# Kernel optimization log

Measured on AMD Instinct MI355X. Metric: run time of the kernel, lower is better.

## Reference

```python
import jax, jax.numpy as jnp
import numpy as np
import math

B, T, C, H = 2, 2048, 512, 8
K, DIL = 3, 1
EPS = 1e-5


def _ln(x, g, b):
    m = jnp.mean(x, axis=-1, keepdims=True)
    v = jnp.mean(jnp.square(x - m), axis=-1, keepdims=True)
    return (x - m) * jax.lax.rsqrt(v + EPS) * g + b


def setup_inputs() -> dict:
    key = jax.random.key(0)
    ks = jax.random.split(key, 12)
    s = 0.02
    return {
        "x": jax.random.normal(ks[0], (B, T, C), jnp.float32),
        "conv_w": jax.random.normal(ks[1], (C, C, K), jnp.float32) * s,  # OIH
        "conv_b": jax.random.normal(ks[2], (C,), jnp.float32) * s,
        "g1": jnp.ones((C,), jnp.float32), "b1": jnp.zeros((C,), jnp.float32),
        "qkv_w": jax.random.normal(ks[3], (C, 3 * C), jnp.float32) * s,
        "qkv_b": jax.random.normal(ks[4], (3 * C,), jnp.float32) * s,
        "proj_w": jax.random.normal(ks[5], (C, C), jnp.float32) * s,
        "proj_b": jax.random.normal(ks[6], (C,), jnp.float32) * s,
        "g2": jnp.ones((C,), jnp.float32), "b2": jnp.zeros((C,), jnp.float32),
        "ffn_w1": jax.random.normal(ks[7], (C, 2 * C), jnp.float32) * s,
        "ffn_b1": jax.random.normal(ks[8], (2 * C,), jnp.float32) * s,
        "ffn_w2": jax.random.normal(ks[9], (2 * C, C), jnp.float32) * s,
        "ffn_b2": jax.random.normal(ks[10], (C,), jnp.float32) * s,
        "g3": jnp.ones((C,), jnp.float32), "b3": jnp.zeros((C,), jnp.float32),
    }


def reference(x, conv_w, conv_b, g1, b1, qkv_w, qkv_b, proj_w, proj_b,
              g2, b2, ffn_w1, ffn_b1, ffn_w2, ffn_b2, g3, b3):
    b, t, c = x.shape
    hd = c // H
    # --- causal dilated conv (left-pad only == pad both + right-trim) ---
    pad = (K - 1) * DIL
    xc = jnp.transpose(x, (0, 2, 1))  # [B,C,T]
    conv = jax.lax.conv_general_dilated(
        xc, conv_w, window_strides=(1,), padding=[(pad, 0)],
        rhs_dilation=(DIL,), dimension_numbers=("NCH", "OIH", "NCH"))
    conv = conv + conv_b[None, :, None]
    x = _ln(x + jnp.transpose(conv, (0, 2, 1)), g1, b1)
    # --- causal self-attention ---
    qkv = (x @ qkv_w + qkv_b).reshape(b, t, 3, H, hd)
    qkv = jnp.transpose(qkv, (2, 0, 3, 1, 4))  # [3,B,H,T,hd]
    q, k, v = qkv[0], qkv[1], qkv[2]
    scores = jnp.einsum("bhqd,bhkd->bhqk", q, k) / math.sqrt(hd)
    causal = jnp.tril(jnp.ones((t, t), bool))
    scores = jnp.where(causal, scores, -jnp.inf)
    attn = jax.nn.softmax(scores, axis=-1)
    out = jnp.einsum("bhqk,bhkd->bhqd", attn, v)
    out = jnp.transpose(out, (0, 2, 1, 3)).reshape(b, t, c)
    out = out @ proj_w + proj_b
    x = _ln(x + out, g2, b2)
    # --- FFN ---
    ffn = jax.nn.relu(x @ ffn_w1 + ffn_b1) @ ffn_w2 + ffn_b2
    return _ln(x + ffn, g3, b3)
```

## Files before the change

kernel.cpp:

```cpp
#include <hip/hip_runtime.h>
#include <hip/hip_bf16.h>

#define TT 2048

typedef __attribute__((ext_vector_type(4))) float f32x4;
typedef __attribute__((ext_vector_type(8))) __bf16 bf16x8;
typedef __attribute__((ext_vector_type(4))) short short4v;
typedef __attribute__((ext_vector_type(8))) short short8v;

enum { M_CONV = 0, M_QKV = 1, M_PROJ = 2, M_FFN1 = 3, M_FFN2 = 4 };

__device__ __forceinline__ void gload16(const void* g, void* l) {
    __builtin_amdgcn_global_load_lds(
        (__attribute__((address_space(1))) void*)g,
        (__attribute__((address_space(3))) void*)l, 16, 0, 0);
}

__device__ __forceinline__ short f2bf(float f) {
    unsigned u = __float_as_uint(f);
    u = (u + 0x7fffu + ((u >> 16) & 1u)) >> 16;
    return (short)u;
}

__device__ __forceinline__ float bf2f(short s) {
    unsigned u = ((unsigned)(unsigned short)s) << 16;
    return __uint_as_float(u);
}

__global__ __launch_bounds__(256) void prep_all(
    const float* __restrict__ conv_w, const float* __restrict__ x,
    const float* __restrict__ qkv_w, const float* __restrict__ proj_w,
    const float* __restrict__ f1w, const float* __restrict__ f2w,
    short* __restrict__ cwT, short* __restrict__ xpad,
    short* __restrict__ qkvT, short* __restrict__ projT,
    short* __restrict__ f1T, short* __restrict__ f2T) {
    if (blockIdx.x < 2048) {
        int t = blockIdx.x;
        const float* src; short* dst; int K, N, lt;
        if (t < 768)       { src = qkv_w;  dst = qkvT;  K = 512;  N = 1536; lt = t; }
        else if (t < 1024) { src = proj_w; dst = projT; K = 512;  N = 512;  lt = t - 768; }
        else if (t < 1536) { src = f1w;    dst = f1T;   K = 512;  N = 1024; lt = t - 1024; }
        else               { src = f2w;    dst = f2T;   K = 1024; N = 512;  lt = t - 1536; }
        int ntn = N >> 5;
        int kt = lt / ntn, nt = lt - kt * ntn;
        int k0 = kt * 32, n0 = nt * 32;
        __shared__ float tile[32][33];
        int c = threadIdx.x & 31, r = threadIdx.x >> 5;
        #pragma unroll
        for (int i = 0; i < 4; i++)
            tile[r + i * 8][c] = src[(size_t)(k0 + r + i * 8) * N + n0 + c];
        __syncthreads();
        #pragma unroll
        for (int i = 0; i < 4; i++)
            dst[(size_t)(n0 + r + i * 8) * K + k0 + c] = f2bf(tile[c][r + i * 8]);
        return;
    }
    int idx = (blockIdx.x - 2048) * 256 + threadIdx.x;
    if (idx < 786432) {
        int tap = idx >> 18, i = (idx >> 9) & 511, o = idx & 511;
        cwT[(size_t)o * 1536 + tap * 512 + i] = f2bf(conv_w[((size_t)o * 512 + i) * 3 + tap]);
        return;
    }
    idx -= 786432;
    if (idx < 2099200) {
        int i = idx & 511, rp = idx >> 9;
        int bb = rp / 2050, rr = rp - bb * 2050;
        int t = rr - 2;
        float v = (t >= 0) ? x[((size_t)(bb << 11) + t) * 512 + i] : 0.f;
        xpad[((size_t)bb * 2050 + rr) * 512 + i] = f2bf(v);
    }
}

__global__ __launch_bounds__(512) void ln_row(const float* __restrict__ in,
                                              const float* __restrict__ g,
                                              const float* __restrict__ b,
                                              float* __restrict__ outf,
                                              short* __restrict__ outb) {
    int row = blockIdx.x * 8 + (threadIdx.x >> 6);
    int l = threadIdx.x & 63;
    const float* p = in + (size_t)row * 512 + l * 8;
    f32x4 v0 = *(const f32x4*)p;
    f32x4 v1 = *(const f32x4*)(p + 4);
    float s = 0.f, ss = 0.f;
    #pragma unroll
    for (int i = 0; i < 4; i++) { s += v0[i]; ss += v0[i] * v0[i]; }
    #pragma unroll
    for (int i = 0; i < 4; i++) { s += v1[i]; ss += v1[i] * v1[i]; }
    #pragma unroll
    for (int off = 1; off < 64; off <<= 1) {
        s  += __shfl_xor(s, off);
        ss += __shfl_xor(ss, off);
    }
    float mean = s * (1.f / 512);
    float var  = ss * (1.f / 512) - mean * mean;
    float rstd = rsqrtf(var + 1e-5f);
    f32x4 g0 = *(const f32x4*)(g + l * 8), g1 = *(const f32x4*)(g + l * 8 + 4);
    f32x4 b0 = *(const f32x4*)(b + l * 8), b1 = *(const f32x4*)(b + l * 8 + 4);
    f32x4 o0, o1;
    #pragma unroll
    for (int i = 0; i < 4; i++) {
        o0[i] = (v0[i] - mean) * rstd * g0[i] + b0[i];
        o1[i] = (v1[i] - mean) * rstd * g1[i] + b1[i];
    }
    float* q = outf + (size_t)row * 512 + l * 8;
    *(f32x4*)q = o0;
    *(f32x4*)(q + 4) = o1;
    if (outb) {
        short4v p0, p1;
        #pragma unroll
        for (int i = 0; i < 4; i++) { p0[i] = f2bf(o0[i]); p1[i] = f2bf(o1[i]); }
        *(short4v*)(outb + (size_t)row * 512 + l * 8) = p0;
        *(short4v*)(outb + (size_t)row * 512 + l * 8 + 4) = p1;
    }
}

template<int MODE>
__device__ __forceinline__ const short* a_ptr(const short* A, int m0, int r, int kk, int K) {
    if constexpr (MODE == M_CONV) {
        int row = m0 + r;
        int bb = row >> 11, t5 = row & 2047;
        int tap = kk >> 9, k2 = kk & 511;
        return A + ((size_t)(bb * 2050 + t5 + tap) * 512 + k2);
    } else {
        return A + ((size_t)(m0 + r) * K + kk);
    }
}

template<int MODE>
__global__ __launch_bounds__(128) void gemm_mfma(
    const short* __restrict__ A, const short* __restrict__ Bw,
    const float* __restrict__ bias, const float* __restrict__ res,
    void* __restrict__ Cout, short* __restrict__ vTb, int K) {
    __shared__ short As[64 * 64];
    __shared__ short Bs[64 * 64];
    const int tid = threadIdx.x;
    const int w = tid >> 6, l = tid & 63;
    const int lr = l & 15, lc = l >> 4;
    const int m0 = blockIdx.x * 64, n0 = blockIdx.y * 64;
    f32x4 acc[2][4];
    #pragma unroll
    for (int mf = 0; mf < 2; mf++)
        #pragma unroll
        for (int nf = 0; nf < 4; nf++) acc[mf][nf] = (f32x4){0.f, 0.f, 0.f, 0.f};

    for (int k0 = 0; k0 < K; k0 += 64) {
        #pragma unroll
        for (int i = 0; i < 4; i++) {
            int u = i * 128 + tid;
            int r = u >> 3, c = (u & 7) ^ (r & 7);
            gload16(a_ptr<MODE>(A, m0, r, k0 + c * 8, K), (char*)As + u * 16);
            gload16(Bw + ((size_t)(n0 + r) * K + k0 + c * 8), (char*)Bs + u * 16);
        }
        __syncthreads();
        bf16x8 af[2][2], bfv[4][2];
        #pragma unroll
        for (int mf = 0; mf < 2; mf++)
            #pragma unroll
            for (int ks = 0; ks < 2; ks++) {
                int rr = w * 32 + mf * 16 + lr;
                int cc = (ks * 4 + lc) ^ (rr & 7);
                af[mf][ks] = *(const bf16x8*)&As[rr * 64 + cc * 8];
            }
        #pragma unroll
        for (int nf = 0; nf < 4; nf++)
            #pragma unroll
            for (int ks = 0; ks < 2; ks++) {
                int rr = nf * 16 + lr;
                int cc = (ks * 4 + lc) ^ (rr & 7);
                bfv[nf][ks] = *(const bf16x8*)&Bs[rr * 64 + cc * 8];
            }
        __builtin_amdgcn_s_setprio(1);
        #pragma unroll
        for (int nf = 0; nf < 4; nf++)
            #pragma unroll
            for (int ks = 0; ks < 2; ks++)
                #pragma unroll
                for (int mf = 0; mf < 2; mf++)
                    acc[mf][nf] = __builtin_amdgcn_mfma_f32_16x16x32_bf16(
                        af[mf][ks], bfv[nf][ks], acc[mf][nf], 0, 0, 0);
        __builtin_amdgcn_s_setprio(0);
        __syncthreads();
    }
    #pragma unroll
    for (int mf = 0; mf < 2; mf++) {
        int row0 = m0 + w * 32 + mf * 16 + lc * 4;
        #pragma unroll
        for (int nf = 0; nf < 4; nf++) {
            int col = n0 + nf * 16 + lr;
            float bv = bias[col];
            if constexpr (MODE == M_CONV || MODE == M_PROJ || MODE == M_FFN2) {
                float* Cf = (float*)Cout;
                #pragma unroll
                for (int rg = 0; rg < 4; rg++) {
                    size_t off = (size_t)(row0 + rg) * 512 + col;
                    Cf[off] = acc[mf][nf][rg] + bv + res[off];
                }
            } else if constexpr (MODE == M_FFN1) {
                short* Cb = (short*)Cout;
                #pragma unroll
                for (int rg = 0; rg < 4; rg++)
                    Cb[(size_t)(row0 + rg) * 1024 + col] =
                        f2bf(fmaxf(acc[mf][nf][rg] + bv, 0.f));
            } else {
                short* Cb = (short*)Cout;
                float v[4];
                #pragma unroll
                for (int rg = 0; rg < 4; rg++) {
                    v[rg] = acc[mf][nf][rg] + bv;
                    Cb[(size_t)(row0 + rg) * 1536 + col] = f2bf(v[rg]);
                }
                if (col >= 1024) {
                    int vc = col - 1024, hh = vc >> 6, dd = vc & 63;
                    int bb = row0 >> 11, t5 = row0 & 2047;
                    short4v pk = {f2bf(v[0]), f2bf(v[1]), f2bf(v[2]), f2bf(v[3])};
                    *(short4v*)&vTb[((size_t)((bb << 3) + hh) * 64 + dd) * 2048 + t5] = pk;
                }
            }
        }
    }
}

__global__ __launch_bounds__(256) void attn_part(const short* __restrict__ qkvb,
                                                 const short* __restrict__ vTb,
                                                 short* __restrict__ pO,
                                                 float* __restrict__ pML) {
    __shared__ short SM[20992];
    const int tid = threadIdx.x;
    const int w = tid >> 6, l = tid & 63;
    const int lr = l & 15, lc = l >> 4;
    const int L = blockIdx.x;
    const int bh = L & 15;
    const int par = (L >> 4) & 1;
    const int qt = 31 - (L >> 5);
    const int b = bh >> 3, h = bh & 7;
    const int qr = w * 16, q0 = qt * 64;
    const int pbase = 16384 + w * (16 * 72);
    const int ntiles = (qt >= par) ? ((qt - par) >> 1) + 1 : 0;

    #pragma unroll
    for (int i = 0; i < 2; i++) {
        int u = i * 256 + tid, r = u >> 3, c = (u & 7) ^ (r & 7);
        gload16(qkvb + ((size_t)(b * 2048 + q0 + r) * 1536 + h * 64 + c * 8),
                (char*)&SM[16384] + u * 16);
        if (ntiles > 0) {
            gload16(qkvb + ((size_t)(b * 2048 + par * 64 + r) * 1536 + 512 + h * 64 + c * 8),
                    (char*)&SM[0] + u * 16);
            gload16(vTb + ((size_t)(bh * 64 + r) * 2048 + par * 64 + c * 8),
                    (char*)&SM[8192] + u * 16);
        }
    }
    __syncthreads();
    bf16x8 aq[2];
    #pragma unroll
    for (int ks = 0; ks < 2; ks++) {
        int rr = qr + lr;
        int cc = (lc + 4 * ks) ^ (rr & 7);
        aq[ks] = *(const bf16x8*)&SM[16384 + rr * 64 + cc * 8];
    }
    __syncthreads();

    f32x4 o[4];
    float mst[4], lst[4];
    #pragma unroll
    for (int nf = 0; nf < 4; nf++) o[nf] = (f32x4){0.f, 0.f, 0.f, 0.f};
    #pragma unroll
    for (int rg = 0; rg < 4; rg++) { mst[rg] = -1e30f; lst[rg] = 0.f; }

    for (int s = 0; s < ntiles; s++) {
        const int kt = par + 2 * s;
        const int cur = s & 1;
        if (s + 1 < ntiles) {
            int ktn = kt + 2, nb = (cur ^ 1) * 4096;
            #pragma unroll
            for (int i = 0; i < 2; i++) {
                int u = i * 256 + tid, r = u >> 3, c = (u & 7) ^ (r & 7);
                gload16(qkvb + ((size_t)(b * 2048 + ktn * 64 + r) * 1536 + 512 + h * 64 + c * 8),
                        (char*)&SM[nb] + u * 16);
                gload16(vTb + ((size_t)(bh * 64 + r) * 2048 + ktn * 64 + c * 8),
                        (char*)&SM[8192 + nb] + u * 16);
            }
        }
        f32x4 s4[4];
        #pragma unroll
        for (int nf = 0; nf < 4; nf++) s4[nf] = (f32x4){0.f, 0.f, 0.f, 0.f};
        __builtin_amdgcn_s_setprio(1);
        #pragma unroll
        for (int nf = 0; nf < 4; nf++) {
            #pragma unroll
            for (int ks = 0; ks < 2; ks++) {
                int rr = nf * 16 + lr;
                int cc = (lc + 4 * ks) ^ (rr & 7);
                bf16x8 bk = *(const bf16x8*)&SM[cur * 4096 + rr * 64 + cc * 8];
                s4[nf] = __builtin_amdgcn_mfma_f32_16x16x32_bf16(aq[ks], bk, s4[nf], 0, 0, 0);
            }
        }
        __builtin_amdgcn_s_setprio(0);
        const bool diag = (kt == qt);
        #pragma unroll
        for (int nf = 0; nf < 4; nf++) {
            #pragma unroll
            for (int rg = 0; rg < 4; rg++) {
                float v = s4[nf][rg] * 0.125f;
                if (diag && (nf * 16 + lr > qr + lc * 4 + rg)) v = -1e30f;
                s4[nf][rg] = v;
            }
        }
        float rm[4];
        int ok = 1;
        #pragma unroll
        for (int rg = 0; rg < 4; rg++) {
            float m_ = fmaxf(fmaxf(s4[0][rg], s4[1][rg]), fmaxf(s4[2][rg], s4[3][rg]));
            m_ = fmaxf(m_, __shfl_xor(m_, 1));
            m_ = fmaxf(m_, __shfl_xor(m_, 2));
            m_ = fmaxf(m_, __shfl_xor(m_, 4));
            m_ = fmaxf(m_, __shfl_xor(m_, 8));
            rm[rg] = m_;
            ok &= (m_ <= mst[rg] + 8.f);
        }
        if (!__all(ok)) {
            #pragma unroll
            for (int rg = 0; rg < 4; rg++) {
                float mn = fmaxf(mst[rg], rm[rg]);
                float alpha = __expf(mst[rg] - mn);
                mst[rg] = mn;
                lst[rg] *= alpha;
                #pragma unroll
                for (int nf = 0; nf < 4; nf++) o[nf][rg] *= alpha;
            }
        }
        #pragma unroll
        for (int rg = 0; rg < 4; rg++) {
            float p0 = __expf(s4[0][rg] - mst[rg]);
            float p1 = __expf(s4[1][rg] - mst[rg]);
            float p2 = __expf(s4[2][rg] - mst[rg]);
            float p3 = __expf(s4[3][rg] - mst[rg]);
            int prow = pbase + (lc * 4 + rg) * 72;
            SM[prow      + lr] = f2bf(p0);
            SM[prow + 16 + lr] = f2bf(p1);
            SM[prow + 32 + lr] = f2bf(p2);
            SM[prow + 48 + lr] = f2bf(p3);
            float rs = p0 + p1 + p2 + p3;
            rs += __shfl_xor(rs, 1);
            rs += __shfl_xor(rs, 2);
            rs += __shfl_xor(rs, 4);
            rs += __shfl_xor(rs, 8);
            lst[rg] += rs;
        }
        bf16x8 pa[2];
        #pragma unroll
        for (int ks = 0; ks < 2; ks++)
            pa[ks] = *(const bf16x8*)&SM[pbase + lr * 72 + ks * 32 + lc * 8];
        __builtin_amdgcn_s_setprio(1);
        #pragma unroll
        for (int nf = 0; nf < 4; nf++) {
            #pragma unroll
            for (int ks = 0; ks < 2; ks++) {
                int rr = nf * 16 + lr;
                int cc = (lc + 4 * ks) ^ (rr & 7);
                bf16x8 bv = *(const bf16x8*)&SM[8192 + cur * 4096 + rr * 64 + cc * 8];
                o[nf] = __builtin_amdgcn_mfma_f32_16x16x32_bf16(pa[ks], bv, o[nf], 0, 0, 0);
            }
        }
        __builtin_amdgcn_s_setprio(0);
        __syncthreads();
    }

    size_t ob = (size_t)L * 4096;
    #pragma unroll
    for (int nf = 0; nf < 4; nf++) {
        #pragma unroll
        for (int rg = 0; rg < 4; rg++) {
            int rw = qr + lc * 4 + rg;
            pO[ob + rw * 64 + nf * 16 + lr] = (ntiles > 0) ? f2bf(o[nf][rg]) : (short)0;
        }
    }
    if (lr == 0) {
        #pragma unroll
        for (int rg = 0; rg < 4; rg++) {
            int rw = qr + lc * 4 + rg;
            pML[(size_t)L * 128 + rw]      = (ntiles > 0) ? mst[rg] : -1e30f;
            pML[(size_t)L * 128 + 64 + rw] = (ntiles > 0) ? lst[rg] : 0.f;
        }
    }
}

__global__ __launch_bounds__(256) void attn_merge(const short* __restrict__ pO,
                                                  const float* __restrict__ pML,
                                                  short* __restrict__ aout) {
    int U = blockIdx.x;
    int bh = U & 15, qt = U >> 4;
    int b = bh >> 3, h = bh & 7, q0 = qt * 64;
    int L0 = ((31 - qt) << 5) | bh;
    int L1 = L0 | 16;
    int t = threadIdx.x;
    int r = t >> 2, cs = (t & 3) * 16;
    float m0 = pML[(size_t)L0 * 128 + r], l0 = pML[(size_t)L0 * 128 + 64 + r];
    float m1 = pML[(size_t)L1 * 128 + r], l1 = pML[(size_t)L1 * 128 + 64 + r];
    float mn = fmaxf(m0, m1);
    float a0 = __expf(m0 - mn), a1 = __expf(m1 - mn);
    float inv = 1.f / (l0 * a0 + l1 * a1);
    #pragma unroll
    for (int half = 0; half < 2; half++) {
        int c0 = cs + half * 8;
        short8v o0 = *(const short8v*)&pO[(size_t)L0 * 4096 + r * 64 + c0];
        short8v o1 = *(const short8v*)&pO[(size_t)L1 * 4096 + r * 64 + c0];
        short8v ov;
        #pragma unroll
        for (int j = 0; j < 8; j++)
            ov[j] = f2bf((bf2f(o0[j]) * a0 + bf2f(o1[j]) * a1) * inv);
        *(short8v*)&aout[(size_t)(b * 2048 + q0 + r) * 512 + h * 64 + c0] = ov;
    }
}

extern "C" void kernel_launch(void* const* d_in, const int* in_sizes, int n_in,
                              void* d_out, int out_size, void* d_ws, size_t ws_size,
                              hipStream_t stream) {
    const float* x      = (const float*)d_in[0];
    const float* conv_w = (const float*)d_in[1];
    const float* conv_b = (const float*)d_in[2];
    const float* g1     = (const float*)d_in[3];
    const float* b1     = (const float*)d_in[4];
    const float* qkv_w  = (const float*)d_in[5];
    const float* qkv_b  = (const float*)d_in[6];
    const float* proj_w = (const float*)d_in[7];
    const float* proj_b = (const float*)d_in[8];
    const float* g2     = (const float*)d_in[9];
    const float* b2     = (const float*)d_in[10];
    const float* ffn_w1 = (const float*)d_in[11];
    const float* ffn_b1 = (const float*)d_in[12];
    const float* ffn_w2 = (const float*)d_in[13];
    const float* ffn_b2 = (const float*)d_in[14];
    const float* g3     = (const float*)d_in[15];
    const float* b3     = (const float*)d_in[16];
    float* out = (float*)d_out;

    char* p = (char*)d_ws;
    short* cwT   = (short*)p;  p += 786432 * 2;
    short* qkvT  = (short*)p;  p += 786432 * 2;
    short* projT = (short*)p;  p += 262144 * 2;
    short* f1T   = (short*)p;  p += 524288 * 2;
    short* f2T   = (short*)p;  p += 524288 * 2;
    short* xpad  = (short*)p;  p += 2099200 * 2;
    float* yb    = (float*)p;  p += 2097152 * 4;
    float* x1f   = (float*)p;  p += 2097152 * 4;
    short* x1b   = (short*)p;  p += 2097152 * 2;
    short* qkvb  = (short*)p;  p += 6291456 * 2;
    short* vTb   = (short*)p;  p += 2097152 * 2;
    short* pO    = (short*)p;  p += 4194304 * 2;
    float* pML   = (float*)p;  p += 131072 * 4;
    float* x2f     = x1f;
    short* x2b     = x1b;
    short* attnout = xpad;
    short* hb      = qkvb;

    prep_all<<<13320, 256, 0, stream>>>(conv_w, x, qkv_w, proj_w, ffn_w1, ffn_w2,
                                        cwT, xpad, qkvT, projT, f1T, f2T);
    gemm_mfma<M_CONV><<<dim3(64, 8), 128, 0, stream>>>(
        xpad, cwT, conv_b, x, yb, nullptr, 1536);
    ln_row<<<512, 512, 0, stream>>>(yb, g1, b1, x1f, x1b);
    gemm_mfma<M_QKV><<<dim3(64, 24), 128, 0, stream>>>(
        x1b, qkvT, qkv_b, nullptr, qkvb, vTb, 512);
    attn_part<<<1024, 256, 0, stream>>>(qkvb, vTb, pO, pML);
    attn_merge<<<512, 256, 0, stream>>>(pO, pML, attnout);
    gemm_mfma<M_PROJ><<<dim3(64, 8), 128, 0, stream>>>(
        attnout, projT, proj_b, x1f, yb, nullptr, 512);
    ln_row<<<512, 512, 0, stream>>>(yb, g2, b2, x2f, x2b);
    gemm_mfma<M_FFN1><<<dim3(64, 16), 128, 0, stream>>>(
        x2b, f1T, ffn_b1, nullptr, hb, nullptr, 512);
    gemm_mfma<M_FFN2><<<dim3(64, 8), 128, 0, stream>>>(
        hb, f2T, ffn_b2, x2f, yb, nullptr, 1024);
    ln_row<<<512, 512, 0, stream>>>(yb, g3, b3, out, nullptr);
}
```

Measured before the change: 141.1 us.

## Fold softmax scale into Q, use exp2, compute row sums via MFMA

```diff
diff --git a/kernel.cpp b/kernel.cpp
--- a/kernel.cpp
+++ b/kernel.cpp
@@ -2,6 +2,7 @@
 #include <hip/hip_bf16.h>
 
 #define TT 2048
+#define QSC 0.18033688011112042f
 
 typedef __attribute__((ext_vector_type(4))) float f32x4;
 typedef __attribute__((ext_vector_type(8))) __bf16 bf16x8;
@@ -207,7 +208,8 @@
                 #pragma unroll
                 for (int rg = 0; rg < 4; rg++) {
                     v[rg] = acc[mf][nf][rg] + bv;
-                    Cb[(size_t)(row0 + rg) * 1536 + col] = f2bf(v[rg]);
+                    float wv = (col < 512) ? v[rg] * QSC : v[rg];
+                    Cb[(size_t)(row0 + rg) * 1536 + col] = f2bf(wv);
                 }
                 if (col >= 1024) {
                     int vc = col - 1024, hh = vc >> 6, dd = vc & 63;
@@ -225,6 +227,7 @@
                                                  short* __restrict__ pO,
                                                  float* __restrict__ pML) {
     __shared__ short SM[20992];
+    __bf16* SMb = (__bf16*)SM;
     const int tid = threadIdx.x;
     const int w = tid >> 6, l = tid & 63;
     const int lr = l & 15, lc = l >> 4;
@@ -259,12 +262,17 @@
     }
     __syncthreads();
 
-    f32x4 o[4];
-    float mst[4], lst[4];
+    bf16x8 onesf;
+    #pragma unroll
+    for (int i = 0; i < 8; i++) onesf[i] = (__bf16)1.0f;
+
+    f32x4 o[4], lacc;
+    float mst[4];
     #pragma unroll
     for (int nf = 0; nf < 4; nf++) o[nf] = (f32x4){0.f, 0.f, 0.f, 0.f};
-    #pragma unroll
-    for (int rg = 0; rg < 4; rg++) { mst[rg] = -1e30f; lst[rg] = 0.f; }
+    lacc = (f32x4){0.f, 0.f, 0.f, 0.f};
+    #pragma unroll
+    for (int rg = 0; rg < 4; rg++) mst[rg] = -1e30f;
 
     for (int s = 0; s < ntiles; s++) {
         const int kt = par + 2 * s;
@@ -296,14 +304,12 @@
         }
         __builtin_amdgcn_s_setprio(0);
         const bool diag = (kt == qt);
-        #pragma unroll
-        for (int nf = 0; nf < 4; nf++) {
-            #pragma unroll
-            for (int rg = 0; rg < 4; rg++) {
-                float v = s4[nf][rg] * 0.125f;
-                if (diag && (nf * 16 + lr > qr + lc * 4 + rg)) v = -1e30f;
-                s4[nf][rg] = v;
-            }
+        if (diag) {
+            #pragma unroll
+            for (int nf = 0; nf < 4; nf++)
+                #pragma unroll
+                for (int rg = 0; rg < 4; rg++)
+                    if (nf * 16 + lr > qr + lc * 4 + rg) s4[nf][rg] = -1e30f;
         }
         float rm[4];
         int ok = 1;
@@ -315,42 +321,35 @@
             m_ = fmaxf(m_, __shfl_xor(m_, 4));
             m_ = fmaxf(m_, __shfl_xor(m_, 8));
             rm[rg] = m_;
-            ok &= (m_ <= mst[rg] + 8.f);
+            ok &= (m_ <= mst[rg] + 11.5f);
         }
         if (!__all(ok)) {
             #pragma unroll
             for (int rg = 0; rg < 4; rg++) {
                 float mn = fmaxf(mst[rg], rm[rg]);
-                float alpha = __expf(mst[rg] - mn);
+                float alpha = exp2f(mst[rg] - mn);
                 mst[rg] = mn;
-                lst[rg] *= alpha;
+                lacc[rg] *= alpha;
                 #pragma unroll
                 for (int nf = 0; nf < 4; nf++) o[nf][rg] *= alpha;
             }
         }
         #pragma unroll
         for (int rg = 0; rg < 4; rg++) {
-            float p0 = __expf(s4[0][rg] - mst[rg]);
-            float p1 = __expf(s4[1][rg] - mst[rg]);
-            float p2 = __expf(s4[2][rg] - mst[rg]);
-            float p3 = __expf(s4[3][rg] - mst[rg]);
             int prow = pbase + (lc * 4 + rg) * 72;
-            SM[prow      + lr] = f2bf(p0);
-            SM[prow + 16 + lr] = f2bf(p1);
-            SM[prow + 32 + lr] = f2bf(p2);
-            SM[prow + 48 + lr] = f2bf(p3);
-            float rs = p0 + p1 + p2 + p3;
-            rs += __shfl_xor(rs, 1);
-            rs += __shfl_xor(rs, 2);
-            rs += __shfl_xor(rs, 4);
-            rs += __shfl_xor(rs, 8);
-            lst[rg] += rs;
+            SMb[prow      + lr] = (__bf16)exp2f(s4[0][rg] - mst[rg]);
+            SMb[prow + 16 + lr] = (__bf16)exp2f(s4[1][rg] - mst[rg]);
+            SMb[prow + 32 + lr] = (__bf16)exp2f(s4[2][rg] - mst[rg]);
+            SMb[prow + 48 + lr] = (__bf16)exp2f(s4[3][rg] - mst[rg]);
         }
         bf16x8 pa[2];
         #pragma unroll
         for (int ks = 0; ks < 2; ks++)
             pa[ks] = *(const bf16x8*)&SM[pbase + lr * 72 + ks * 32 + lc * 8];
         __builtin_amdgcn_s_setprio(1);
+        #pragma unroll
+        for (int ks = 0; ks < 2; ks++)
+            lacc = __builtin_amdgcn_mfma_f32_16x16x32_bf16(pa[ks], onesf, lacc, 0, 0, 0);
         #pragma unroll
         for (int nf = 0; nf < 4; nf++) {
             #pragma unroll
@@ -379,7 +378,7 @@
         for (int rg = 0; rg < 4; rg++) {
             int rw = qr + lc * 4 + rg;
             pML[(size_t)L * 128 + rw]      = (ntiles > 0) ? mst[rg] : -1e30f;
-            pML[(size_t)L * 128 + 64 + rw] = (ntiles > 0) ? lst[rg] : 0.f;
+            pML[(size_t)L * 128 + 64 + rw] = (ntiles > 0) ? lacc[rg] : 0.f;
         }
     }
 }
@@ -397,7 +396,7 @@
     float m0 = pML[(size_t)L0 * 128 + r], l0 = pML[(size_t)L0 * 128 + 64 + r];
     float m1 = pML[(size_t)L1 * 128 + r], l1 = pML[(size_t)L1 * 128 + 64 + r];
     float mn = fmaxf(m0, m1);
-    float a0 = __expf(m0 - mn), a1 = __expf(m1 - mn);
+    float a0 = exp2f(m0 - mn), a1 = exp2f(m1 - mn);
     float inv = 1.f / (l0 * a0 + l1 * a1);
     #pragma unroll
     for (int half = 0; half < 2; half++) {
```

Measured after the change: 135.6 us. 3.9% less time.
